# Kernel optimization log

Hardware: AMD Instinct MI355X
Metric: run time of the kernel (lower is better)

The kernel has to match this reference:

```python
import jax, jax.numpy as jnp
import numpy as np

NUM_HEADS = 4
LN_EPS = 1e-5


def rotate_half(x):
    x1 = x[..., ::2]
    x2 = x[..., 1::2]
    return jnp.stack((-x2, x1), axis=-1).reshape(x.shape)


def apply_rope(freqs, t):
    # freqs: [2, B, 1, S, hd] (cos, sin); t: [B, H, S, hd]
    return t * freqs[0] + rotate_half(t) * freqs[1]


def normalize_kpts(kpts):
    size = 1.0 + kpts.max(-2) - kpts.min(-2)          # [B, 2]
    shift = size / 2.0
    scale = size.max(-1) / 2.0                         # [B]
    return (kpts - shift[..., None, :]) / scale[..., None, None]


def posenc(kpts, Wr):
    proj = kpts @ Wr                                   # [B, S, hd//2]
    emb = jnp.stack([jnp.cos(proj), jnp.sin(proj)], 0)[:, :, None, :, :]  # [2,B,1,S,hd//2]
    return jnp.repeat(emb, 2, axis=-1)                 # [2, B, 1, S, hd]


def layer_norm(x, g, b):
    mu = x.mean(-1, keepdims=True)
    var = ((x - mu) ** 2).mean(-1, keepdims=True)
    return (x - mu) / jnp.sqrt(var + LN_EPS) * g + b


def ffn(x, W1, b1, g, bt, W2, b2):
    return jax.nn.gelu(layer_norm(x @ W1 + b1, g, bt), approximate=False) @ W2 + b2


def heads_split(t, H):  # [B,S,D] -> [B,H,S,hd]
    B, S, D = t.shape
    return t.reshape(B, S, H, D // H).transpose(0, 2, 1, 3)


def heads_merge(t):  # [B,H,S,hd] -> [B,S,D]
    B, H, S, hd = t.shape
    return t.transpose(0, 2, 1, 3).reshape(B, S, H * hd)


def self_block(x, enc, Wqkv, bqkv, Wo, bo, W1, b1, g, bt, W2, b2):
    B, S, D = x.shape
    H = NUM_HEADS
    hd = D // H
    qkv = (x @ Wqkv + bqkv).reshape(B, S, H, hd, 3).transpose(0, 2, 1, 3, 4)
    q, k, v = qkv[..., 0], qkv[..., 1], qkv[..., 2]
    q = apply_rope(enc, q)
    k = apply_rope(enc, k)
    sim = jnp.einsum('bhid,bhjd->bhij', q, k) * (hd ** -0.5)
    ctx = jnp.einsum('bhij,bhjd->bhid', jax.nn.softmax(sim, axis=-1), v)
    msg = heads_merge(ctx) @ Wo + bo
    return x + ffn(jnp.concatenate([x, msg], axis=-1), W1, b1, g, bt, W2, b2)


def cross_block(x0, x1, Wqk, bqk, Wv, bv, Wo, bo, W1, b1, g, bt, W2, b2):
    H = NUM_HEADS
    hd = x0.shape[-1] // H
    qk0 = heads_split(x0 @ Wqk + bqk, H)
    qk1 = heads_split(x1 @ Wqk + bqk, H)
    v0 = heads_split(x0 @ Wv + bv, H)
    v1 = heads_split(x1 @ Wv + bv, H)
    sc = hd ** -0.25  # scale**0.5 applied to each of qk0, qk1
    sim = jnp.einsum('bhid,bhjd->bhij', qk0 * sc, qk1 * sc)
    m0 = jnp.einsum('bhij,bhjd->bhid', jax.nn.softmax(sim, axis=-1), v1)
    m1 = jnp.einsum('bhij,bhid->bhjd', jax.nn.softmax(sim, axis=-2), v0)
    m0 = heads_merge(m0) @ Wo + bo
    m1 = heads_merge(m1) @ Wo + bo
    x0 = x0 + ffn(jnp.concatenate([x0, m0], axis=-1), W1, b1, g, bt, W2, b2)
    x1 = x1 + ffn(jnp.concatenate([x1, m1], axis=-1), W1, b1, g, bt, W2, b2)
    return x0, x1


def setup_inputs() -> dict:
    key = jax.random.key(0)
    ks = iter(jax.random.split(key, 64))
    B, M, N, D, L = 2, 1024, 1024, 256, 9
    hd = D // NUM_HEADS
    def nrm(shape, scale):
        return jax.random.normal(next(ks), shape, jnp.float32) * scale
    s = 1.0 / np.sqrt(D)
    s2 = 1.0 / np.sqrt(2 * D)
    return {
        'kpts0': jax.random.uniform(next(ks), (B, M, 2), jnp.float32) * 1024.0,
        'kpts1': jax.random.uniform(next(ks), (B, N, 2), jnp.float32) * 1024.0,
        'desc0': nrm((B, M, D), 1.0),
        'desc1': nrm((B, N, D), 1.0),
        'Wr': nrm((2, hd // 2), 1.0),
        'Win': nrm((D, D), s), 'b_in': jnp.zeros(D),
        'sWqkv': nrm((L, D, 3 * D), s), 'sbqkv': jnp.zeros((L, 3 * D)),
        'sWo': nrm((L, D, D), s), 'sbo': jnp.zeros((L, D)),
        'sW1': nrm((L, 2 * D, 2 * D), s2), 'sb1': jnp.zeros((L, 2 * D)),
        'sg': jnp.ones((L, 2 * D)), 'sbt': jnp.zeros((L, 2 * D)),
        'sW2': nrm((L, 2 * D, D), s2), 'sb2': jnp.zeros((L, D)),
        'cWqk': nrm((L, D, D), s), 'cbqk': jnp.zeros((L, D)),
        'cWv': nrm((L, D, D), s), 'cbv': jnp.zeros((L, D)),
        'cWo': nrm((L, D, D), s), 'cbo': jnp.zeros((L, D)),
        'cW1': nrm((L, 2 * D, 2 * D), s2), 'cb1': jnp.zeros((L, 2 * D)),
        'cg': jnp.ones((L, 2 * D)), 'cbt': jnp.zeros((L, 2 * D)),
        'cW2': nrm((L, 2 * D, D), s2), 'cb2': jnp.zeros((L, D)),
        'Wf': nrm((D, D), s), 'bf': jnp.zeros(D),
        'Wlv': nrm((D, 2), s), 'blv': jnp.zeros(2),
    }


def reference(kpts0, kpts1, desc0, desc1, Wr, Win, b_in,
              sWqkv, sbqkv, sWo, sbo, sW1, sb1, sg, sbt, sW2, sb2,
              cWqk, cbqk, cWv, cbv, cWo, cbo, cW1, cb1, cg, cbt, cW2, cb2,
              Wf, bf, Wlv, blv):
    enc0 = posenc(normalize_kpts(kpts0), Wr)
    enc1 = posenc(normalize_kpts(kpts1), Wr)
    x0 = desc0 @ Win + b_in
    x1 = desc1 @ Win + b_in
    for l in range(sWqkv.shape[0]):
        x0 = self_block(x0, enc0, sWqkv[l], sbqkv[l], sWo[l], sbo[l],
                        sW1[l], sb1[l], sg[l], sbt[l], sW2[l], sb2[l])
        x1 = self_block(x1, enc1, sWqkv[l], sbqkv[l], sWo[l], sbo[l],
                        sW1[l], sb1[l], sg[l], sbt[l], sW2[l], sb2[l])
        x0, x1 = cross_block(x0, x1, cWqk[l], cbqk[l], cWv[l], cbv[l], cWo[l], cbo[l],
                             cW1[l], cb1[l], cg[l], cbt[l], cW2[l], cb2[l])
    d = x0.shape[-1]
    md0 = (x0 @ Wf + bf) / d ** 0.25
    md1 = (x1 @ Wf + bf) / d ** 0.25
    sim = jnp.einsum('bmd,bnd->bmn', md0, md1)
    p_rp_01 = jax.nn.softmax(sim, axis=-1)
    p_rp_10 = jax.nn.softmax(sim, axis=-2)  # == softmax(sim^T, -1)^T
    logvar_01 = x0 @ Wlv + blv
    logvar_10 = x1 @ Wlv + blv
    return (p_rp_01, p_rp_10, logvar_01, logvar_10)
```

## Files before the change

### kernel.cpp

```cpp
#include <hip/hip_runtime.h>
#include <hip/hip_bf16.h>
#include <math.h>

using bf16 = __hip_bfloat16;
typedef __attribute__((ext_vector_type(8))) short short8;
typedef __attribute__((ext_vector_type(4))) float f32x4;

__device__ __forceinline__ float bf2f(bf16 x){ return __bfloat162float(x); }
__device__ __forceinline__ bf16  f2bf(float x){ return __float2bfloat16(x); }
__device__ __forceinline__ float ldin(const void* p, size_t i, int f){
  return f ? ((const float*)p)[i] : bf2f(((const bf16*)p)[i]);
}
__device__ __forceinline__ void stout(void* out, size_t i, float v, int f){
  if (f) ((float*)out)[i] = v; else ((bf16*)out)[i] = f2bf(v);
}
__device__ __forceinline__ void split2(float v, bf16* hi, bf16* lo){
  bf16 h = f2bf(v); *hi = h; *lo = f2bf(v - bf2f(h));
}
#define MFMA(a, b, c) __builtin_amdgcn_mfma_f32_16x16x32_bf16(a, b, c, 0, 0, 0)

__global__ void sniff_kernel(const unsigned* __restrict__ sg, int* __restrict__ flag)
{
  if (threadIdx.x == 0 && blockIdx.x == 0) *flag = (sg[0] == 0x3F800000u) ? 1 : 0;
}

__global__ __launch_bounds__(256) void cvtf_kernel(const void* __restrict__ src, float* __restrict__ dst,
                                                   int n, const int* __restrict__ flag)
{
  int f = *flag;
  int i = blockIdx.x * 256 + threadIdx.x;
  if (i < n) dst[i] = ldin(src, i, f);
}

__global__ __launch_bounds__(256) void splitin_kernel(const void* __restrict__ src,
                                                      bf16* __restrict__ hi, bf16* __restrict__ lo,
                                                      int n, const int* __restrict__ flag)
{
  int f = *flag;
  int i = blockIdx.x * 256 + threadIdx.x;
  if (i < n) split2(ldin(src, i, f), &hi[i], &lo[i]);
}

template<bool ADDC>
__global__ __launch_bounds__(256) void gemm2_kernel(
    const bf16* __restrict__ Ahi, const bf16* __restrict__ Alo,
    const bf16* __restrict__ Bhi, const bf16* __restrict__ Blo,
    float* __restrict__ C, bf16* __restrict__ Chi, bf16* __restrict__ Clo,
    const float* __restrict__ bias,
    int K, int lda, int ldb, int ldc, int ldcp,
    long sAb, long sBb, long sCb, float scale)
{
  int z = blockIdx.z;
  Ahi += (size_t)z * sAb; Alo += (size_t)z * sAb;
  Bhi += (size_t)z * sBb; Blo += (size_t)z * sBb;
  size_t coff = (size_t)z * sCb;
  const int bm = blockIdx.y * 64, bn = blockIdx.x * 64;
  __shared__ bf16 AsH[64][72], AsL[64][72], BsH[64][72], BsL[64][72];
  const int tid  = threadIdx.x;
  const int lane = tid & 63, wid = tid >> 6;
  const int wr = wid >> 1, wc = wid & 1;
  const int srow = tid >> 2, sch = (tid & 3) * 8;
  const int lr = lane & 15, kg = (lane >> 4) * 8;
  f32x4 zero = {0.f, 0.f, 0.f, 0.f};
  f32x4 acc[2][2] = {{zero, zero}, {zero, zero}};
  for (int kt = 0; kt < K; kt += 64) {
    __syncthreads();
    size_t arow = (size_t)(bm + srow) * lda + kt + sch;
    size_t brow = (size_t)(bn + srow) * ldb + kt + sch;
    *(short8*)&AsH[srow][sch]      = *(const short8*)&Ahi[arow];
    *(short8*)&AsH[srow][sch + 32] = *(const short8*)&Ahi[arow + 32];
    *(short8*)&AsL[srow][sch]      = *(const short8*)&Alo[arow];
    *(short8*)&AsL[srow][sch + 32] = *(const short8*)&Alo[arow + 32];
    *(short8*)&BsH[srow][sch]      = *(const short8*)&Bhi[brow];
    *(short8*)&BsH[srow][sch + 32] = *(const short8*)&Bhi[brow + 32];
    *(short8*)&BsL[srow][sch]      = *(const short8*)&Blo[brow];
    *(short8*)&BsL[srow][sch + 32] = *(const short8*)&Blo[brow + 32];
    __syncthreads();
    #pragma unroll
    for (int kk = 0; kk < 2; kk++) {
      int kc = kk * 32 + kg;
      short8 ah0 = *(const short8*)&AsH[wr * 32 + lr][kc];
      short8 ah1 = *(const short8*)&AsH[wr * 32 + 16 + lr][kc];
      short8 al0 = *(const short8*)&AsL[wr * 32 + lr][kc];
      short8 al1 = *(const short8*)&AsL[wr * 32 + 16 + lr][kc];
      short8 bh0 = *(const short8*)&BsH[wc * 32 + lr][kc];
      short8 bh1 = *(const short8*)&BsH[wc * 32 + 16 + lr][kc];
      short8 bl0 = *(const short8*)&BsL[wc * 32 + lr][kc];
      short8 bl1 = *(const short8*)&BsL[wc * 32 + 16 + lr][kc];
      acc[0][0] = MFMA(ah0, bh0, acc[0][0]);
      acc[0][1] = MFMA(ah0, bh1, acc[0][1]);
      acc[1][0] = MFMA(ah1, bh0, acc[1][0]);
      acc[1][1] = MFMA(ah1, bh1, acc[1][1]);
      acc[0][0] = MFMA(ah0, bl0, acc[0][0]);
      acc[0][1] = MFMA(ah0, bl1, acc[0][1]);
      acc[1][0] = MFMA(ah1, bl0, acc[1][0]);
      acc[1][1] = MFMA(ah1, bl1, acc[1][1]);
      acc[0][0] = MFMA(al0, bh0, acc[0][0]);
      acc[0][1] = MFMA(al0, bh1, acc[0][1]);
      acc[1][0] = MFMA(al1, bh0, acc[1][0]);
      acc[1][1] = MFMA(al1, bh1, acc[1][1]);
    }
  }
  #pragma unroll
  for (int i = 0; i < 2; i++)
    #pragma unroll
    for (int j = 0; j < 2; j++) {
      int col = bn + wc * 32 + j * 16 + lr;
      float bv = bias ? bias[col] : 0.f;
      #pragma unroll
      for (int r = 0; r < 4; r++) {
        int row = bm + wr * 32 + i * 16 + (lane >> 4) * 4 + r;
        float v = (acc[i][j][r] + bv) * scale;
        if (C) {
          size_t idx = coff + (size_t)row * ldc + col;
          if (ADDC) v += C[idx];
          C[idx] = v;
        }
        if (Chi) {
          size_t idxp = (size_t)row * ldcp + col;
          split2(v, &Chi[idxp], &Clo[idxp]);
        }
      }
    }
}

template<bool ADDC>
static void gemm2(hipStream_t st, const bf16* Ahi, const bf16* Alo, const bf16* Bhi, const bf16* Blo,
                  float* C, bf16* Chi, bf16* Clo, const float* bias,
                  int M, int N, int K, int lda, int ldb, int ldc, int ldcp,
                  int Z, long sAb, long sBb, long sCb, float scale)
{
  dim3 g(N / 64, M / 64, Z);
  gemm2_kernel<ADDC><<<g, 256, 0, st>>>(Ahi, Alo, Bhi, Blo, C, Chi, Clo, bias,
                                        K, lda, ldb, ldc, ldcp, sAb, sBb, sCb, scale);
}

__global__ __launch_bounds__(256) void fattn_kernel(
    const bf16* __restrict__ Qh, const bf16* __restrict__ Ql,
    const bf16* __restrict__ Kh, const bf16* __restrict__ Kl,
    const bf16* __restrict__ Vh, const bf16* __restrict__ Vl,
    bf16* __restrict__ Oh, bf16* __restrict__ Ol,
    int ldq, int ldo, int cross, float scale)
{
  const int S = 1024;
  int z = blockIdx.y;
  size_t qoff, koff, voff, ooff;
  if (!cross) {
    qoff = (size_t)z * S * 64; koff = qoff;
    voff = (size_t)z * 64 * S;
    ooff = (size_t)(z >> 2) * S * 256 + (size_t)(z & 3) * 64;
  } else {
    int dir = z >> 3, b = (z >> 2) & 1, h = z & 3;
    size_t off0 = (size_t)b * S * 256 + (size_t)h * 64;
    size_t off1 = (size_t)(2048 + b * 1024) * 256 + (size_t)h * 64;
    if (dir == 0) { qoff = off0; koff = off1; voff = (size_t)(8 + b * 4 + h) * 64 * S; ooff = off0; }
    else          { qoff = off1; koff = off0; voff = (size_t)(b * 4 + h) * 64 * S;     ooff = off1; }
  }
  __shared__ bf16 KsH[64][72], KsL[64][72], VsH[64][72], VsL[64][72];
  __shared__ bf16 PsH[4][16][72], PsL[4][16][72];
  const int tid = threadIdx.x;
  const int lane = tid & 63, w = tid >> 6;
  const int lr = lane & 15, kg8 = (lane >> 4) * 8;
  const int q0 = blockIdx.x * 64;
  int qrow = q0 + (w << 4) + lr;
  short8 aQh[2], aQl[2];
  #pragma unroll
  for (int kk = 0; kk < 2; kk++) {
    size_t qi = qoff + (size_t)qrow * ldq + kk * 32 + kg8;
    aQh[kk] = *(const short8*)&Qh[qi];
    aQl[kk] = *(const short8*)&Ql[qi];
  }
  f32x4 zero = {0.f, 0.f, 0.f, 0.f};
  f32x4 accO[4] = {zero, zero, zero, zero};
  float m[4] = {-1e30f, -1e30f, -1e30f, -1e30f};
  float l[4] = {0.f, 0.f, 0.f, 0.f};
  const int srow = tid >> 2, sch = (tid & 3) * 8;
  for (int kt = 0; kt < 16; kt++) {
    __syncthreads();
    size_t ki = koff + (size_t)(kt * 64 + srow) * ldq + sch;
    size_t vi = voff + (size_t)srow * S + kt * 64 + sch;
    *(short8*)&KsH[srow][sch]      = *(const short8*)&Kh[ki];
    *(short8*)&KsH[srow][sch + 32] = *(const short8*)&Kh[ki + 32];
    *(short8*)&KsL[srow][sch]      = *(const short8*)&Kl[ki];
    *(short8*)&KsL[srow][sch + 32] = *(const short8*)&Kl[ki + 32];
    *(short8*)&VsH[srow][sch]      = *(const short8*)&Vh[vi];
    *(short8*)&VsH[srow][sch + 32] = *(const short8*)&Vh[vi + 32];
    *(short8*)&VsL[srow][sch]      = *(const short8*)&Vl[vi];
    *(short8*)&VsL[srow][sch + 32] = *(const short8*)&Vl[vi + 32];
    __syncthreads();
    f32x4 s[4] = {zero, zero, zero, zero};
    #pragma unroll
    for (int kk = 0; kk < 2; kk++)
      #pragma unroll
      for (int j = 0; j < 4; j++) {
        short8 bh = *(const short8*)&KsH[j * 16 + lr][kk * 32 + kg8];
        short8 bl = *(const short8*)&KsL[j * 16 + lr][kk * 32 + kg8];
        s[j] = MFMA(aQh[kk], bh, s[j]);
        s[j] = MFMA(aQh[kk], bl, s[j]);
        s[j] = MFMA(aQl[kk], bh, s[j]);
      }
    float fac[4], rs[4];
    #pragma unroll
    for (int r = 0; r < 4; r++) {
      float v = fmaxf(fmaxf(s[0][r], s[1][r]), fmaxf(s[2][r], s[3][r])) * scale;
      #pragma unroll
      for (int o = 8; o; o >>= 1) v = fmaxf(v, __shfl_xor(v, o));
      float nm = fmaxf(m[r], v);
      fac[r] = expf(m[r] - nm);
      m[r] = nm;
      rs[r] = 0.f;
    }
    #pragma unroll
    for (int j = 0; j < 4; j++)
      #pragma unroll
      for (int r = 0; r < 4; r++) {
        float p = expf(s[j][r] * scale - m[r]);
        s[j][r] = p;
        rs[r] += p;
      }
    #pragma unroll
    for (int r = 0; r < 4; r++) {
      float v = rs[r];
      #pragma unroll
      for (int o = 8; o; o >>= 1) v += __shfl_xor(v, o);
      l[r] = l[r] * fac[r] + v;
      #pragma unroll
      for (int n = 0; n < 4; n++) accO[n][r] *= fac[r];
    }
    #pragma unroll
    for (int j = 0; j < 4; j++)
      #pragma unroll
      for (int r = 0; r < 4; r++)
        split2(s[j][r], &PsH[w][(lane >> 4) * 4 + r][j * 16 + lr],
                        &PsL[w][(lane >> 4) * 4 + r][j * 16 + lr]);
    __syncthreads();
    #pragma unroll
    for (int kk = 0; kk < 2; kk++) {
      short8 pah = *(const short8*)&PsH[w][lr][kk * 32 + kg8];
      short8 pal = *(const short8*)&PsL[w][lr][kk * 32 + kg8];
      #pragma unroll
      for (int n = 0; n < 4; n++) {
        short8 vh = *(const short8*)&VsH[n * 16 + lr][kk * 32 + kg8];
        short8 vl = *(const short8*)&VsL[n * 16 + lr][kk * 32 + kg8];
        accO[n] = MFMA(pah, vh, accO[n]);
        accO[n] = MFMA(pah, vl, accO[n]);
        accO[n] = MFMA(pal, vh, accO[n]);
      }
    }
  }
  #pragma unroll
  for (int n = 0; n < 4; n++)
    #pragma unroll
    for (int r = 0; r < 4; r++) {
      float v = accO[n][r] / l[r];
      int row = q0 + (w << 4) + (lane >> 4) * 4 + r;
      int col = n * 16 + lr;
      size_t idx = ooff + (size_t)row * ldo + col;
      split2(v, &Oh[idx], &Ol[idx]);
    }
}

__global__ __launch_bounds__(256) void transpose2_kernel(const void* __restrict__ src,
                                                         bf16* __restrict__ dhi, bf16* __restrict__ dlo,
                                                         int R, int C, const int* __restrict__ flag)
{
  __shared__ float tile[32][33];
  int f = *flag;
  size_t zoff = (size_t)blockIdx.z * R * C;
  int c0 = blockIdx.x * 32, r0 = blockIdx.y * 32;
  int x = threadIdx.x, y = threadIdx.y;
  for (int i = y; i < 32; i += 8)
    tile[i][x] = ldin(src, zoff + (size_t)(r0 + i) * C + (c0 + x), f);
  __syncthreads();
  for (int i = y; i < 32; i += 8) {
    size_t di = zoff + (size_t)(c0 + i) * R + (r0 + x);
    split2(tile[x][i], &dhi[di], &dlo[di]);
  }
}

__global__ __launch_bounds__(256) void minmax_kernel(const void* __restrict__ k0,
                                                     const void* __restrict__ k1,
                                                     float* __restrict__ mm, const int* __restrict__ flag)
{
  int f = *flag;
  int z = blockIdx.x;
  const void* kp = (z >= 2) ? k1 : k0;
  size_t base = (size_t)(z & 1) * 1024 * 2;
  int t = threadIdx.x;
  float mnx = 1e30f, mxx = -1e30f, mny = 1e30f, mxy = -1e30f;
  for (int s = t; s < 1024; s += 256) {
    float x = ldin(kp, base + s * 2, f), y = ldin(kp, base + s * 2 + 1, f);
    mnx = fminf(mnx, x); mxx = fmaxf(mxx, x);
    mny = fminf(mny, y); mxy = fmaxf(mxy, y);
  }
  for (int o = 32; o; o >>= 1) {
    mnx = fminf(mnx, __shfl_xor(mnx, o)); mxx = fmaxf(mxx, __shfl_xor(mxx, o));
    mny = fminf(mny, __shfl_xor(mny, o)); mxy = fmaxf(mxy, __shfl_xor(mxy, o));
  }
  __shared__ float r[4][4];
  if ((t & 63) == 0) { int w = t >> 6; r[w][0] = mnx; r[w][1] = mxx; r[w][2] = mny; r[w][3] = mxy; }
  __syncthreads();
  if (t == 0) {
    for (int w = 1; w < 4; w++) {
      r[0][0] = fminf(r[0][0], r[w][0]); r[0][1] = fmaxf(r[0][1], r[w][1]);
      r[0][2] = fminf(r[0][2], r[w][2]); r[0][3] = fmaxf(r[0][3], r[w][3]);
    }
    mm[z * 4 + 0] = r[0][0]; mm[z * 4 + 1] = r[0][1]; mm[z * 4 + 2] = r[0][2]; mm[z * 4 + 3] = r[0][3];
  }
}

__global__ __launch_bounds__(256) void posenc_kernel(const void* __restrict__ k0, const void* __restrict__ k1,
                                                     const float* __restrict__ mm, const void* __restrict__ Wr,
                                                     float* __restrict__ ecos, float* __restrict__ esin,
                                                     const int* __restrict__ flag)
{
  int f = *flag;
  int idx = blockIdx.x * 256 + threadIdx.x;
  int z = idx >> 10;
  const void* kp = (z >= 2) ? k1 : k0;
  size_t base = (size_t)(z & 1) * 1024 * 2 + (size_t)(idx & 1023) * 2;
  float sx = 1.f + mm[z * 4 + 1] - mm[z * 4 + 0];
  float sy = 1.f + mm[z * 4 + 3] - mm[z * 4 + 2];
  float scale = fmaxf(sx, sy) * 0.5f;
  float xn = (ldin(kp, base, f)     - sx * 0.5f) / scale;
  float yn = (ldin(kp, base + 1, f) - sy * 0.5f) / scale;
  for (int j = 0; j < 32; j++) {
    float p = xn * ldin(Wr, j, f) + yn * ldin(Wr, 32 + j, f);
    ecos[(size_t)idx * 32 + j] = cosf(p);
    esin[(size_t)idx * 32 + j] = sinf(p);
  }
}

__global__ __launch_bounds__(256) void rope_kernel(const float* __restrict__ qkv,
                                                   const float* __restrict__ ecos, const float* __restrict__ esin,
                                                   bf16* __restrict__ qh, bf16* __restrict__ ql,
                                                   bf16* __restrict__ kh, bf16* __restrict__ kl,
                                                   bf16* __restrict__ vh, bf16* __restrict__ vl)
{
  int idx = blockIdx.x * 256 + threadIdx.x;
  int row = idx >> 5, p = idx & 31;
  int zz = row >> 10, s = row & 1023;
  float c  = ecos[(size_t)row * 32 + p];
  float sn = esin[(size_t)row * 32 + p];
  const float* qp = qkv + (size_t)row * 768;
  #pragma unroll
  for (int h = 0; h < 4; h++) {
    int base = h * 192 + p * 6;
    float q0 = qp[base + 0], k0 = qp[base + 1], v0 = qp[base + 2];
    float q1 = qp[base + 3], k1 = qp[base + 4], v1 = qp[base + 5];
    int zh = zz * 4 + h;
    size_t qo = ((size_t)zh * 1024 + s) * 64 + 2 * p;
    split2(q0 * c - q1 * sn, &qh[qo],     &ql[qo]);
    split2(q1 * c + q0 * sn, &qh[qo + 1], &ql[qo + 1]);
    split2(k0 * c - k1 * sn, &kh[qo],     &kl[qo]);
    split2(k1 * c + k0 * sn, &kh[qo + 1], &kl[qo + 1]);
    size_t vo = ((size_t)zh * 64 + 2 * p) * 1024 + s;
    split2(v0, &vh[vo],        &vl[vo]);
    split2(v1, &vh[vo + 1024], &vl[vo + 1024]);
  }
}

__global__ __launch_bounds__(256) void vsplitT_kernel(const bf16* __restrict__ vhi, const bf16* __restrict__ vlo,
                                                      bf16* __restrict__ vThi, bf16* __restrict__ vTlo)
{
  __shared__ bf16 tile[32][33];
  int zz = blockIdx.z >> 1, plane = blockIdx.z & 1;
  const bf16* v  = plane ? vlo  : vhi;
  bf16*       vT = plane ? vTlo : vThi;
  int h = blockIdx.y >> 1, d0 = (blockIdx.y & 1) * 32;
  int s0 = blockIdx.x * 32;
  int x = threadIdx.x, y = threadIdx.y;
  const bf16* sp = v + ((size_t)zz * 1024 + s0) * 256 + h * 64 + d0;
  for (int i = y; i < 32; i += 8) tile[i][x] = sp[(size_t)i * 256 + x];
  __syncthreads();
  bf16* dp = vT + (((size_t)(zz * 4 + h)) * 64 + d0) * 1024 + s0;
  for (int i = y; i < 32; i += 8) dp[(size_t)i * 1024 + x] = tile[x][i];
}

__global__ __launch_bounds__(256) void row_softmax_kernel(const float* __restrict__ in,
                                                          void* __restrict__ outp, size_t eoff,
                                                          const int* __restrict__ flagp)
{
  int f = *flagp;
  size_t row = blockIdx.x;
  const float* ip = in + row * 1024;
  int t = threadIdx.x;
  float v[4]; float mx = -1e30f;
  #pragma unroll
  for (int i = 0; i < 4; i++) { v[i] = ip[t + i * 256]; mx = fmaxf(mx, v[i]); }
  #pragma unroll
  for (int o = 32; o; o >>= 1) mx = fmaxf(mx, __shfl_xor(mx, o));
  __shared__ float red[4];
  if ((t & 63) == 0) red[t >> 6] = mx;
  __syncthreads();
  mx = fmaxf(fmaxf(red[0], red[1]), fmaxf(red[2], red[3]));
  float sm = 0.f;
  #pragma unroll
  for (int i = 0; i < 4; i++) { v[i] = expf(v[i] - mx); sm += v[i]; }
  #pragma unroll
  for (int o = 32; o; o >>= 1) sm += __shfl_xor(sm, o);
  __shared__ float red2[4];
  if ((t & 63) == 0) red2[t >> 6] = sm;
  __syncthreads();
  sm = red2[0] + red2[1] + red2[2] + red2[3];
  float inv = 1.f / sm;
  size_t ob = eoff + row * 1024;
  #pragma unroll
  for (int i = 0; i < 4; i++) stout(outp, ob + t + i * 256, v[i] * inv, f);
}

__global__ __launch_bounds__(256) void col_softmax_kernel(const float* __restrict__ sim, void* __restrict__ out,
                                                          size_t eoff, const int* __restrict__ flagp)
{
  int f = *flagp;
  int b = blockIdx.y;
  int tid = threadIdx.x;
  int lane = tid & 63, w = tid >> 6;
  int lc = tid & 15;
  int g  = tid >> 4;
  int c = blockIdx.x * 16 + lc;
  const float* sp = sim + (size_t)b * 1048576 + c;
  float mx = -1e30f;
  for (int r = g; r < 1024; r += 16) mx = fmaxf(mx, sp[(size_t)r * 1024]);
  mx = fmaxf(mx, __shfl_xor(mx, 16));
  mx = fmaxf(mx, __shfl_xor(mx, 32));
  __shared__ float redm[4][16], reds[4][16];
  if ((lane >> 4) == 0) redm[w][lc] = mx;
  __syncthreads();
  mx = fmaxf(fmaxf(redm[0][lc], redm[1][lc]), fmaxf(redm[2][lc], redm[3][lc]));
  float sm = 0.f;
  for (int r = g; r < 1024; r += 16) sm += expf(sp[(size_t)r * 1024] - mx);
  sm += __shfl_xor(sm, 16);
  sm += __shfl_xor(sm, 32);
  if ((lane >> 4) == 0) reds[w][lc] = sm;
  __syncthreads();
  sm = reds[0][lc] + reds[1][lc] + reds[2][lc] + reds[3][lc];
  float inv = 1.f / sm;
  size_t ob = eoff + (size_t)b * 1048576 + c;
  for (int r = g; r < 1024; r += 16)
    stout(out, ob + (size_t)r * 1024, expf(sp[(size_t)r * 1024] - mx) * inv, f);
}

__global__ __launch_bounds__(256) void ln_gelu_kernel(const bf16* __restrict__ hh, const bf16* __restrict__ hl,
                                                      bf16* __restrict__ oh, bf16* __restrict__ ol,
                                                      const float* __restrict__ g, const float* __restrict__ bt)
{
  size_t row = blockIdx.x;
  const bf16 *hp = hh + row * 512, *lp = hl + row * 512;
  int t = threadIdx.x;
  float a = bf2f(hp[t]) + bf2f(lp[t]);
  float b = bf2f(hp[t + 256]) + bf2f(lp[t + 256]);
  float s = a + b, s2 = a * a + b * b;
  #pragma unroll
  for (int o = 32; o; o >>= 1) { s += __shfl_xor(s, o); s2 += __shfl_xor(s2, o); }
  __shared__ float r1[4], r2[4];
  if ((t & 63) == 0) { r1[t >> 6] = s; r2[t >> 6] = s2; }
  __syncthreads();
  s = r1[0] + r1[1] + r1[2] + r1[3];
  s2 = r2[0] + r2[1] + r2[2] + r2[3];
  float mu = s * (1.f / 512.f);
  float var = s2 * (1.f / 512.f) - mu * mu;
  float inv = rsqrtf(var + 1e-5f);
  float o1 = (a - mu) * inv * g[t] + bt[t];
  float o2 = (b - mu) * inv * g[t + 256] + bt[t + 256];
  o1 = 0.5f * o1 * (1.f + erff(o1 * 0.70710678118f));
  o2 = 0.5f * o2 * (1.f + erff(o2 * 0.70710678118f));
  split2(o1, &oh[row * 512 + t],       &ol[row * 512 + t]);
  split2(o2, &oh[row * 512 + t + 256], &ol[row * 512 + t + 256]);
}

__global__ __launch_bounds__(256) void logvar_kernel(const float* __restrict__ x, const void* __restrict__ Wlv,
                                                     const void* __restrict__ blv, void* __restrict__ out,
                                                     size_t eoff, const int* __restrict__ flagp)
{
  int f = *flagp;
  int idx = blockIdx.x * 256 + threadIdx.x;
  int r = idx >> 1, c = idx & 1;
  float acc = ldin(blv, c, f);
  const float* xp = x + (size_t)r * 256;
  for (int d = 0; d < 256; d++) acc += xp[d] * ldin(Wlv, d * 2 + c, f);
  int img = r >> 11, rs = r & 2047;
  stout(out, eoff + (size_t)img * 4096 + rs * 2 + c, acc, f);
}

extern "C" void kernel_launch(void* const* d_in, const int* in_sizes, int n_in,
                              void* d_out, int out_size, void* d_ws, size_t ws_size,
                              hipStream_t stream)
{
  (void)in_sizes; (void)n_in; (void)out_size; (void)ws_size;
  const int L = 9, S = 1024;
  const long SS = (long)S * S;
  char* w = (char*)d_ws; size_t off = 0;
  auto alloc = [&](size_t bytes) -> void* {
    void* p = w + off; off = (off + bytes + 1023) & ~(size_t)1023; return p;
  };
  struct Pair { bf16 *hi, *lo; };
  auto apair = [&](size_t elems) -> Pair {
    Pair p; p.hi = (bf16*)alloc(elems * 2); p.lo = (bf16*)alloc(elems * 2); return p;
  };
  int*   flag  = (int*)alloc(4);
  float* mm    = (float*)alloc(16 * 4);
  float* b_in  = (float*)alloc(256 * 4);
  float* sbqkv = (float*)alloc((size_t)L * 768 * 4);
  float* sbo   = (float*)alloc((size_t)L * 256 * 4);
  float* sb1   = (float*)alloc((size_t)L * 512 * 4);
  float* sg    = (float*)alloc((size_t)L * 512 * 4);
  float* sbt   = (float*)alloc((size_t)L * 512 * 4);
  float* sb2   = (float*)alloc((size_t)L * 256 * 4);
  float* cbqk  = (float*)alloc((size_t)L * 256 * 4);
  float* cbv   = (float*)alloc((size_t)L * 256 * 4);
  float* cbo   = (float*)alloc((size_t)L * 256 * 4);
  float* cb1   = (float*)alloc((size_t)L * 512 * 4);
  float* cg    = (float*)alloc((size_t)L * 512 * 4);
  float* cbt   = (float*)alloc((size_t)L * 512 * 4);
  float* cb2   = (float*)alloc((size_t)L * 256 * 4);
  float* bfv   = (float*)alloc(256 * 4);
  Pair WinT   = apair(65536);
  Pair WfT    = apair(65536);
  Pair sWqkvT = apair((size_t)L * 196608);
  Pair sWoT   = apair((size_t)L * 65536);
  Pair sW1T   = apair((size_t)L * 262144);
  Pair sW2T   = apair((size_t)L * 131072);
  Pair cWqkT  = apair((size_t)L * 65536);
  Pair cWvT   = apair((size_t)L * 65536);
  Pair cWoT   = apair((size_t)L * 65536);
  Pair cW1T   = apair((size_t)L * 262144);
  Pair cW2T   = apair((size_t)L * 131072);
  float* ecos  = (float*)alloc((size_t)4 * S * 32 * 4);
  float* esin  = (float*)alloc((size_t)4 * S * 32 * 4);
  float* xall  = (float*)alloc((size_t)4096 * 256 * 4);
  Pair qP      = apair((size_t)16 * S * 64);
  Pair kP      = apair((size_t)16 * S * 64);
  Pair vTP     = apair((size_t)16 * 64 * S);
  Pair catP    = apair((size_t)4096 * 512);
  Pair hmP     = apair((size_t)4096 * 512);
  Pair ctxP    = apair((size_t)4096 * 256);
  float* qkvb  = (float*)alloc((size_t)4096 * 768 * 4);
  float* simf  = (float*)alloc((size_t)2 * SS * 4);
  bf16* XH = catP.hi;
  bf16* XL = catP.lo;
  Pair qk2P  = {(bf16*)qkvb, (bf16*)qkvb + (size_t)4096 * 256};
  Pair v2P   = {(bf16*)qkvb + (size_t)2 * 4096 * 256, (bf16*)qkvb + (size_t)3 * 4096 * 256};
  Pair xinP  = {(bf16*)qkvb, (bf16*)qkvb + (size_t)4096 * 256};
  Pair mdP   = {(bf16*)qkvb, (bf16*)qkvb + (size_t)4096 * 256};

  sniff_kernel<<<1, 64, 0, stream>>>((const unsigned*)d_in[13], flag);

  auto cvtf = [&](const void* src, float* dst, int n) {
    cvtf_kernel<<<(n + 255) / 256, 256, 0, stream>>>(src, dst, n, flag);
  };
  cvtf(d_in[6],  b_in,  256);
  cvtf(d_in[8],  sbqkv, L * 768);
  cvtf(d_in[10], sbo,   L * 256);
  cvtf(d_in[12], sb1,   L * 512);
  cvtf(d_in[13], sg,    L * 512);
  cvtf(d_in[14], sbt,   L * 512);
  cvtf(d_in[16], sb2,   L * 256);
  cvtf(d_in[18], cbqk,  L * 256);
  cvtf(d_in[20], cbv,   L * 256);
  cvtf(d_in[22], cbo,   L * 256);
  cvtf(d_in[24], cb1,   L * 512);
  cvtf(d_in[25], cg,    L * 512);
  cvtf(d_in[26], cbt,   L * 512);
  cvtf(d_in[28], cb2,   L * 256);
  cvtf(d_in[30], bfv,   256);

  dim3 tb(32, 8);
  transpose2_kernel<<<dim3(8, 8, 1), tb, 0, stream>>>(d_in[5],  WinT.hi,   WinT.lo,   256, 256, flag);
  transpose2_kernel<<<dim3(8, 8, 1), tb, 0, stream>>>(d_in[29], WfT.hi,    WfT.lo,    256, 256, flag);
  transpose2_kernel<<<dim3(24, 8, L), tb, 0, stream>>>(d_in[7],  sWqkvT.hi, sWqkvT.lo, 256, 768, flag);
  transpose2_kernel<<<dim3(8, 8, L), tb, 0, stream>>>(d_in[9],  sWoT.hi,   sWoT.lo,   256, 256, flag);
  transpose2_kernel<<<dim3(16, 16, L), tb, 0, stream>>>(d_in[11], sW1T.hi,  sW1T.lo,  512, 512, flag);
  transpose2_kernel<<<dim3(8, 16, L), tb, 0, stream>>>(d_in[15], sW2T.hi,   sW2T.lo,  512, 256, flag);
  transpose2_kernel<<<dim3(8, 8, L), tb, 0, stream>>>(d_in[17], cWqkT.hi,  cWqkT.lo,  256, 256, flag);
  transpose2_kernel<<<dim3(8, 8, L), tb, 0, stream>>>(d_in[19], cWvT.hi,   cWvT.lo,   256, 256, flag);
  transpose2_kernel<<<dim3(8, 8, L), tb, 0, stream>>>(d_in[21], cWoT.hi,   cWoT.lo,   256, 256, flag);
  transpose2_kernel<<<dim3(16, 16, L), tb, 0, stream>>>(d_in[23], cW1T.hi,  cW1T.lo,  512, 512, flag);
  transpose2_kernel<<<dim3(8, 16, L), tb, 0, stream>>>(d_in[27], cW2T.hi,   cW2T.lo,  512, 256, flag);

  minmax_kernel<<<4, 256, 0, stream>>>(d_in[0], d_in[1], mm, flag);
  posenc_kernel<<<16, 256, 0, stream>>>(d_in[0], d_in[1], mm, d_in[4], ecos, esin, flag);

  splitin_kernel<<<2048, 256, 0, stream>>>(d_in[2], xinP.hi, xinP.lo, 2048 * 256, flag);
  splitin_kernel<<<2048, 256, 0, stream>>>(d_in[3], xinP.hi + (size_t)2048 * 256,
                                           xinP.lo + (size_t)2048 * 256, 2048 * 256, flag);
  gemm2<false>(stream, xinP.hi, xinP.lo, WinT.hi, WinT.lo, xall, XH, XL, b_in,
               4096, 256, 256, 256, 256, 256, 512, 1, 0, 0, 0, 1.f);

  for (int l = 0; l < L; l++) {
    gemm2<false>(stream, XH, XL, sWqkvT.hi + (size_t)l * 196608, sWqkvT.lo + (size_t)l * 196608,
                 qkvb, nullptr, nullptr, sbqkv + l * 768,
                 4096, 768, 256, 512, 256, 768, 0, 1, 0, 0, 0, 1.f);
    rope_kernel<<<512, 256, 0, stream>>>(qkvb, ecos, esin, qP.hi, qP.lo, kP.hi, kP.lo, vTP.hi, vTP.lo);
    fattn_kernel<<<dim3(16, 16), 256, 0, stream>>>(qP.hi, qP.lo, kP.hi, kP.lo, vTP.hi, vTP.lo,
                                                   ctxP.hi, ctxP.lo, 64, 256, 0, 0.125f);
    gemm2<false>(stream, ctxP.hi, ctxP.lo, sWoT.hi + (size_t)l * 65536, sWoT.lo + (size_t)l * 65536,
                 nullptr, catP.hi + 256, catP.lo + 256, sbo + l * 256,
                 4096, 256, 256, 256, 256, 0, 512, 1, 0, 0, 0, 1.f);
    gemm2<false>(stream, catP.hi, catP.lo, sW1T.hi + (size_t)l * 262144, sW1T.lo + (size_t)l * 262144,
                 nullptr, hmP.hi, hmP.lo, sb1 + l * 512,
                 4096, 512, 512, 512, 512, 0, 512, 1, 0, 0, 0, 1.f);
    ln_gelu_kernel<<<4096, 256, 0, stream>>>(hmP.hi, hmP.lo, hmP.hi, hmP.lo, sg + l * 512, sbt + l * 512);
    gemm2<true>(stream, hmP.hi, hmP.lo, sW2T.hi + (size_t)l * 131072, sW2T.lo + (size_t)l * 131072,
                xall, XH, XL, sb2 + l * 256,
                4096, 256, 512, 512, 512, 256, 512, 1, 0, 0, 0, 1.f);

    gemm2<false>(stream, XH, XL, cWqkT.hi + (size_t)l * 65536, cWqkT.lo + (size_t)l * 65536,
                 nullptr, qk2P.hi, qk2P.lo, cbqk + l * 256,
                 4096, 256, 256, 512, 256, 0, 256, 1, 0, 0, 0, 1.f);
    gemm2<false>(stream, XH, XL, cWvT.hi + (size_t)l * 65536, cWvT.lo + (size_t)l * 65536,
                 nullptr, v2P.hi, v2P.lo, cbv + l * 256,
                 4096, 256, 256, 512, 256, 0, 256, 1, 0, 0, 0, 1.f);
    vsplitT_kernel<<<dim3(32, 8, 8), tb, 0, stream>>>(v2P.hi, v2P.lo, vTP.hi, vTP.lo);
    fattn_kernel<<<dim3(16, 16), 256, 0, stream>>>(qk2P.hi, qk2P.lo, qk2P.hi, qk2P.lo, vTP.hi, vTP.lo,
                                                   ctxP.hi, ctxP.lo, 256, 256, 1, 0.125f);
    gemm2<false>(stream, ctxP.hi, ctxP.lo, cWoT.hi + (size_t)l * 65536, cWoT.lo + (size_t)l * 65536,
                 nullptr, catP.hi + 256, catP.lo + 256, cbo + l * 256,
                 4096, 256, 256, 256, 256, 0, 512, 1, 0, 0, 0, 1.f);
    gemm2<false>(stream, catP.hi, catP.lo, cW1T.hi + (size_t)l * 262144, cW1T.lo + (size_t)l * 262144,
                 nullptr, hmP.hi, hmP.lo, cb1 + l * 512,
                 4096, 512, 512, 512, 512, 0, 512, 1, 0, 0, 0, 1.f);
    ln_gelu_kernel<<<4096, 256, 0, stream>>>(hmP.hi, hmP.lo, hmP.hi, hmP.lo, cg + l * 512, cbt + l * 512);
    gemm2<true>(stream, hmP.hi, hmP.lo, cW2T.hi + (size_t)l * 131072, cW2T.lo + (size_t)l * 131072,
                xall, XH, XL, cb2 + l * 256,
                4096, 256, 512, 512, 512, 256, 512, 1, 0, 0, 0, 1.f);
  }

  gemm2<false>(stream, XH, XL, WfT.hi, WfT.lo, nullptr, mdP.hi, mdP.lo, bfv,
               4096, 256, 256, 512, 256, 0, 256, 1, 0, 0, 0, 0.25f);
  gemm2<false>(stream, mdP.hi, mdP.lo, mdP.hi + (size_t)2048 * 256, mdP.lo + (size_t)2048 * 256,
               simf, nullptr, nullptr, nullptr,
               1024, 1024, 256, 256, 256, 1024, 0, 2, (long)1024 * 256, (long)1024 * 256, SS, 1.f);
  row_softmax_kernel<<<2048, 256, 0, stream>>>(simf, d_out, 0, flag);
  col_softmax_kernel<<<dim3(64, 2), 256, 0, stream>>>(simf, d_out, 2097152, flag);
  logvar_kernel<<<32, 256, 0, stream>>>(xall, d_in[31], d_in[32], d_out, 4194304, flag);
}
```

Before: 2.267 ms.

## Add 128x128 split-bf16 GEMM for wide projections and halve attention block size

Adds a 128x128-tile split-precision GEMM kernel (4 waves, each computing a 64x64 subtile) and uses it for the QKV and FFN-up projections, so each block gets more operand reuse out of shared memory. The flash-attention kernel now runs 2 waves per block over 32 query rows instead of 4 waves over 64 rows, which doubles the grid from 256 to 512 blocks to fill more compute units. In exchange, the attention blocks reload each K/V tile for half as many queries, and the larger GEMM tiles give fewer blocks for the N=768 and N=512 shapes.

```diff
diff --git a/kernel.cpp b/kernel.cpp
--- a/kernel.cpp
+++ b/kernel.cpp
@@ -135,7 +135,85 @@
                                         K, lda, ldb, ldc, ldcp, sAb, sBb, sCb, scale);
 }
 
-__global__ __launch_bounds__(256) void fattn_kernel(
+__global__ __launch_bounds__(256) void gemm2_128_kernel(
+    const bf16* __restrict__ Ahi, const bf16* __restrict__ Alo,
+    const bf16* __restrict__ Bhi, const bf16* __restrict__ Blo,
+    float* __restrict__ C, bf16* __restrict__ Chi, bf16* __restrict__ Clo,
+    const float* __restrict__ bias,
+    int K, int lda, int ldb, int ldc, int ldcp, float scale)
+{
+  const int bm = blockIdx.y * 128, bn = blockIdx.x * 128;
+  __shared__ bf16 AsH[128][40], AsL[128][40], BsH[128][40], BsL[128][40];
+  const int tid  = threadIdx.x;
+  const int lane = tid & 63, wid = tid >> 6;
+  const int wr = wid >> 1, wc = wid & 1;
+  const int srow = tid >> 1, scol = (tid & 1) * 16;
+  const int lr = lane & 15, kg = (lane >> 4) * 8;
+  f32x4 zero = {0.f, 0.f, 0.f, 0.f};
+  f32x4 acc[4][4];
+  #pragma unroll
+  for (int i = 0; i < 4; i++)
+    #pragma unroll
+    for (int j = 0; j < 4; j++) acc[i][j] = zero;
+  for (int kt = 0; kt < K; kt += 32) {
+    __syncthreads();
+    size_t arow = (size_t)(bm + srow) * lda + kt + scol;
+    size_t brow = (size_t)(bn + srow) * ldb + kt + scol;
+    *(short8*)&AsH[srow][scol]     = *(const short8*)&Ahi[arow];
+    *(short8*)&AsH[srow][scol + 8] = *(const short8*)&Ahi[arow + 8];
+    *(short8*)&AsL[srow][scol]     = *(const short8*)&Alo[arow];
+    *(short8*)&AsL[srow][scol + 8] = *(const short8*)&Alo[arow + 8];
+    *(short8*)&BsH[srow][scol]     = *(const short8*)&Bhi[brow];
+    *(short8*)&BsH[srow][scol + 8] = *(const short8*)&Bhi[brow + 8];
+    *(short8*)&BsL[srow][scol]     = *(const short8*)&Blo[brow];
+    *(short8*)&BsL[srow][scol + 8] = *(const short8*)&Blo[brow + 8];
+    __syncthreads();
+    short8 ah[4], al[4], bh[4], bl[4];
+    #pragma unroll
+    for (int i = 0; i < 4; i++) {
+      ah[i] = *(const short8*)&AsH[wr * 64 + i * 16 + lr][kg];
+      al[i] = *(const short8*)&AsL[wr * 64 + i * 16 + lr][kg];
+      bh[i] = *(const short8*)&BsH[wc * 64 + i * 16 + lr][kg];
+      bl[i] = *(const short8*)&BsL[wc * 64 + i * 16 + lr][kg];
+    }
+    #pragma unroll
+    for (int i = 0; i < 4; i++)
+      #pragma unroll
+      for (int j = 0; j < 4; j++) {
+        acc[i][j] = MFMA(ah[i], bh[j], acc[i][j]);
+        acc[i][j] = MFMA(ah[i], bl[j], acc[i][j]);
+        acc[i][j] = MFMA(al[i], bh[j], acc[i][j]);
+      }
+  }
+  #pragma unroll
+  for (int i = 0; i < 4; i++)
+    #pragma unroll
+    for (int j = 0; j < 4; j++) {
+      int col = bn + wc * 64 + j * 16 + lr;
+      float bv = bias ? bias[col] : 0.f;
+      #pragma unroll
+      for (int r = 0; r < 4; r++) {
+        int row = bm + wr * 64 + i * 16 + (lane >> 4) * 4 + r;
+        float v = (acc[i][j][r] + bv) * scale;
+        if (C) C[(size_t)row * ldc + col] = v;
+        if (Chi) {
+          size_t idxp = (size_t)row * ldcp + col;
+          split2(v, &Chi[idxp], &Clo[idxp]);
+        }
+      }
+    }
+}
+
+static void g128(hipStream_t st, const bf16* Ahi, const bf16* Alo, const bf16* Bhi, const bf16* Blo,
+                 float* C, bf16* Chi, bf16* Clo, const float* bias,
+                 int M, int N, int K, int lda, int ldb, int ldc, int ldcp, float scale)
+{
+  dim3 g(N / 128, M / 128);
+  gemm2_128_kernel<<<g, 256, 0, st>>>(Ahi, Alo, Bhi, Blo, C, Chi, Clo, bias,
+                                      K, lda, ldb, ldc, ldcp, scale);
+}
+
+__global__ __launch_bounds__(128) void fattn_kernel(
     const bf16* __restrict__ Qh, const bf16* __restrict__ Ql,
     const bf16* __restrict__ Kh, const bf16* __restrict__ Kl,
     const bf16* __restrict__ Vh, const bf16* __restrict__ Vl,
@@ -157,11 +235,11 @@
     else          { qoff = off1; koff = off0; voff = (size_t)(b * 4 + h) * 64 * S;     ooff = off1; }
   }
   __shared__ bf16 KsH[64][72], KsL[64][72], VsH[64][72], VsL[64][72];
-  __shared__ bf16 PsH[4][16][72], PsL[4][16][72];
+  __shared__ bf16 PsH[2][16][72], PsL[2][16][72];
   const int tid = threadIdx.x;
   const int lane = tid & 63, w = tid >> 6;
   const int lr = lane & 15, kg8 = (lane >> 4) * 8;
-  const int q0 = blockIdx.x * 64;
+  const int q0 = blockIdx.x * 32;
   int qrow = q0 + (w << 4) + lr;
   short8 aQh[2], aQl[2];
   #pragma unroll
@@ -174,19 +252,18 @@
   f32x4 accO[4] = {zero, zero, zero, zero};
   float m[4] = {-1e30f, -1e30f, -1e30f, -1e30f};
   float l[4] = {0.f, 0.f, 0.f, 0.f};
-  const int srow = tid >> 2, sch = (tid & 3) * 8;
+  const int srow = tid >> 1, sb = (tid & 1) * 32;
   for (int kt = 0; kt < 16; kt++) {
     __syncthreads();
-    size_t ki = koff + (size_t)(kt * 64 + srow) * ldq + sch;
-    size_t vi = voff + (size_t)srow * S + kt * 64 + sch;
-    *(short8*)&KsH[srow][sch]      = *(const short8*)&Kh[ki];
-    *(short8*)&KsH[srow][sch + 32] = *(const short8*)&Kh[ki + 32];
-    *(short8*)&KsL[srow][sch]      = *(const short8*)&Kl[ki];
-    *(short8*)&KsL[srow][sch + 32] = *(const short8*)&Kl[ki + 32];
-    *(short8*)&VsH[srow][sch]      = *(const short8*)&Vh[vi];
-    *(short8*)&VsH[srow][sch + 32] = *(const short8*)&Vh[vi + 32];
-    *(short8*)&VsL[srow][sch]      = *(const short8*)&Vl[vi];
-    *(short8*)&VsL[srow][sch + 32] = *(const short8*)&Vl[vi + 32];
+    size_t ki = koff + (size_t)(kt * 64 + srow) * ldq + sb;
+    size_t vi = voff + (size_t)srow * S + kt * 64 + sb;
+    #pragma unroll
+    for (int c = 0; c < 32; c += 8) {
+      *(short8*)&KsH[srow][sb + c] = *(const short8*)&Kh[ki + c];
+      *(short8*)&KsL[srow][sb + c] = *(const short8*)&Kl[ki + c];
+      *(short8*)&VsH[srow][sb + c] = *(const short8*)&Vh[vi + c];
+      *(short8*)&VsL[srow][sb + c] = *(const short8*)&Vl[vi + c];
+    }
     __syncthreads();
     f32x4 s[4] = {zero, zero, zero, zero};
     #pragma unroll
@@ -588,18 +665,16 @@
                4096, 256, 256, 256, 256, 256, 512, 1, 0, 0, 0, 1.f);
 
   for (int l = 0; l < L; l++) {
-    gemm2<false>(stream, XH, XL, sWqkvT.hi + (size_t)l * 196608, sWqkvT.lo + (size_t)l * 196608,
-                 qkvb, nullptr, nullptr, sbqkv + l * 768,
-                 4096, 768, 256, 512, 256, 768, 0, 1, 0, 0, 0, 1.f);
+    g128(stream, XH, XL, sWqkvT.hi + (size_t)l * 196608, sWqkvT.lo + (size_t)l * 196608,
+         qkvb, nullptr, nullptr, sbqkv + l * 768, 4096, 768, 256, 512, 256, 768, 0, 1.f);
     rope_kernel<<<512, 256, 0, stream>>>(qkvb, ecos, esin, qP.hi, qP.lo, kP.hi, kP.lo, vTP.hi, vTP.lo);
-    fattn_kernel<<<dim3(16, 16), 256, 0, stream>>>(qP.hi, qP.lo, kP.hi, kP.lo, vTP.hi, vTP.lo,
+    fattn_kernel<<<dim3(32, 16), 128, 0, stream>>>(qP.hi, qP.lo, kP.hi, kP.lo, vTP.hi, vTP.lo,
                                                    ctxP.hi, ctxP.lo, 64, 256, 0, 0.125f);
     gemm2<false>(stream, ctxP.hi, ctxP.lo, sWoT.hi + (size_t)l * 65536, sWoT.lo + (size_t)l * 65536,
                  nullptr, catP.hi + 256, catP.lo + 256, sbo + l * 256,
                  4096, 256, 256, 256, 256, 0, 512, 1, 0, 0, 0, 1.f);
-    gemm2<false>(stream, catP.hi, catP.lo, sW1T.hi + (size_t)l * 262144, sW1T.lo + (size_t)l * 262144,
-                 nullptr, hmP.hi, hmP.lo, sb1 + l * 512,
-                 4096, 512, 512, 512, 512, 0, 512, 1, 0, 0, 0, 1.f);
+    g128(stream, catP.hi, catP.lo, sW1T.hi + (size_t)l * 262144, sW1T.lo + (size_t)l * 262144,
+         nullptr, hmP.hi, hmP.lo, sb1 + l * 512, 4096, 512, 512, 512, 512, 0, 512, 1.f);
     ln_gelu_kernel<<<4096, 256, 0, stream>>>(hmP.hi, hmP.lo, hmP.hi, hmP.lo, sg + l * 512, sbt + l * 512);
     gemm2<true>(stream, hmP.hi, hmP.lo, sW2T.hi + (size_t)l * 131072, sW2T.lo + (size_t)l * 131072,
                 xall, XH, XL, sb2 + l * 256,
@@ -612,14 +687,13 @@
                  nullptr, v2P.hi, v2P.lo, cbv + l * 256,
                  4096, 256, 256, 512, 256, 0, 256, 1, 0, 0, 0, 1.f);
     vsplitT_kernel<<<dim3(32, 8, 8), tb, 0, stream>>>(v2P.hi, v2P.lo, vTP.hi, vTP.lo);
-    fattn_kernel<<<dim3(16, 16), 256, 0, stream>>>(qk2P.hi, qk2P.lo, qk2P.hi, qk2P.lo, vTP.hi, vTP.lo,
+    fattn_kernel<<<dim3(32, 16), 128, 0, stream>>>(qk2P.hi, qk2P.lo, qk2P.hi, qk2P.lo, vTP.hi, vTP.lo,
                                                    ctxP.hi, ctxP.lo, 256, 256, 1, 0.125f);
     gemm2<false>(stream, ctxP.hi, ctxP.lo, cWoT.hi + (size_t)l * 65536, cWoT.lo + (size_t)l * 65536,
                  nullptr, catP.hi + 256, catP.lo + 256, cbo + l * 256,
                  4096, 256, 256, 256, 256, 0, 512, 1, 0, 0, 0, 1.f);
-    gemm2<false>(stream, catP.hi, catP.lo, cW1T.hi + (size_t)l * 262144, cW1T.lo + (size_t)l * 262144,
-                 nullptr, hmP.hi, hmP.lo, cb1 + l * 512,
-                 4096, 512, 512, 512, 512, 0, 512, 1, 0, 0, 0, 1.f);
+    g128(stream, catP.hi, catP.lo, cW1T.hi + (size_t)l * 262144, cW1T.lo + (size_t)l * 262144,
+         nullptr, hmP.hi, hmP.lo, cb1 + l * 512, 4096, 512, 512, 512, 512, 0, 512, 1.f);
     ln_gelu_kernel<<<4096, 256, 0, stream>>>(hmP.hi, hmP.lo, hmP.hi, hmP.lo, cg + l * 512, cbt + l * 512);
     gemm2<true>(stream, hmP.hi, hmP.lo, cW2T.hi + (size_t)l * 131072, cW2T.lo + (size_t)l * 131072,
                 xall, XH, XL, cb2 + l * 256,
```

New measurement: 2.776 ms. 1.22x slower.
